# Optimization experiments

Hardware: AMD Instinct MI355X
Metric: run time of the kernel (lower is better)

Reference implementation:

```python
import jax, jax.numpy as jnp
import numpy as np
import math

DIM = 2048
N_HEADS = 16
Q_LORA = 512
KV_LORA = 512
NOPE = 128
ROPE = 64
QK_HD = NOPE + ROPE
V_HD = 128
THETA = 1e6


def _linear_params(key, fan_in, fan_out):
    kw, kb = jax.random.split(key)
    w = jax.random.normal(kw, (fan_in, fan_out), jnp.float32) * 0.02
    b = jax.random.normal(kb, (fan_out,), jnp.float32) * 0.02
    return w, b


def setup_inputs() -> dict:
    key = jax.random.key(0)
    ks = jax.random.split(key, 6)
    x = jax.random.normal(ks[0], (2, 2048, DIM), jnp.float32)
    wq_a_w, wq_a_b = _linear_params(ks[1], DIM, Q_LORA)
    wq_b_w, wq_b_b = _linear_params(ks[2], Q_LORA, N_HEADS * QK_HD)
    wkv_a_w, wkv_a_b = _linear_params(ks[3], DIM, KV_LORA + ROPE)
    wkv_b_w, wkv_b_b = _linear_params(ks[4], KV_LORA, N_HEADS * (NOPE + V_HD))
    wo_w, wo_b = _linear_params(ks[5], N_HEADS * V_HD, DIM)
    return {"x": x,
            "wq_a_w": wq_a_w, "wq_a_b": wq_a_b,
            "wq_b_w": wq_b_w, "wq_b_b": wq_b_b,
            "wkv_a_w": wkv_a_w, "wkv_a_b": wkv_a_b,
            "wkv_b_w": wkv_b_w, "wkv_b_b": wkv_b_b,
            "wo_w": wo_w, "wo_b": wo_b}


def _rope_cos_sin(seq_len):
    # freqs = 1/theta^(2i/ROPE), i in [0, ROPE/2)
    inv_freq = 1.0 / (THETA ** (jnp.arange(0, ROPE, 2, dtype=jnp.float32) / ROPE))
    t = jnp.arange(seq_len, dtype=jnp.float32)
    freqs = jnp.outer(t, inv_freq)  # (S, ROPE/2)
    return jnp.cos(freqs), jnp.sin(freqs)


def _apply_rope(x, cos, sin):
    # x: (B, S, H, ROPE); pairs (even, odd) form complex numbers
    xr = x[..., 0::2]
    xi = x[..., 1::2]
    c = cos[None, :, None, :]
    s = sin[None, :, None, :]
    out_r = xr * c - xi * s
    out_i = xr * s + xi * c
    return jnp.stack([out_r, out_i], axis=-1).reshape(x.shape)


def reference(x, wq_a_w, wq_a_b, wq_b_w, wq_b_b, wkv_a_w, wkv_a_b,
              wkv_b_w, wkv_b_b, wo_w, wo_b):
    bs, seq_len, _ = x.shape
    # low-rank Q projection
    q = (x @ wq_a_w + wq_a_b) @ wq_b_w + wq_b_b
    q = q.reshape(bs, seq_len, N_HEADS, QK_HD)
    q_nope, q_pe = q[..., :NOPE], q[..., NOPE:]
    # compressed KV + decoupled rope key
    ckv = x @ wkv_a_w + wkv_a_b
    compressed_kv, k_pe = ckv[..., :KV_LORA], ckv[..., KV_LORA:]
    k_pe = k_pe.reshape(bs, seq_len, 1, ROPE)
    kv = (compressed_kv @ wkv_b_w + wkv_b_b).reshape(bs, seq_len, N_HEADS, NOPE + V_HD)
    kv_nope, v = kv[..., :NOPE], kv[..., NOPE:]
    # partial RoPE
    cos, sin = _rope_cos_sin(seq_len)
    q_pe = _apply_rope(q_pe, cos, sin)
    k_pe = _apply_rope(k_pe, cos, sin)
    k_pe = jnp.broadcast_to(k_pe, (bs, seq_len, N_HEADS, ROPE))
    qf = jnp.concatenate([q_nope, q_pe], axis=-1)   # (B,S,H,QK_HD)
    kf = jnp.concatenate([kv_nope, k_pe], axis=-1)  # (B,S,H,QK_HD)
    # full attention (no mask, scale by sqrt(v_head_dim) per source)
    scores = jnp.einsum('bqhd,bkhd->bhqk', qf, kf) / math.sqrt(V_HD)
    probs = jax.nn.softmax(scores.astype(jnp.float32), axis=-1).astype(qf.dtype)
    out = jnp.einsum('bhqk,bkhd->bqhd', probs, v)
    out = out.reshape(bs, seq_len, N_HEADS * V_HD)
    return out @ wo_w + wo_b
```

## Files before the change

kernel.cpp:

```cpp
#include <hip/hip_runtime.h>
#include <hip/hip_bf16.h>


typedef __attribute__((ext_vector_type(8))) short short8;
typedef __attribute__((ext_vector_type(4))) short short4v;
typedef __attribute__((ext_vector_type(4))) float f32x4;

#define GLOAD_LDS16(gp, lp)                                                      \
  __builtin_amdgcn_global_load_lds((const __attribute__((address_space(1))) void*)(gp), \
                                   (__attribute__((address_space(3))) void*)(lp), 16, 0, 0)

static __device__ __forceinline__ unsigned short bf16_bits(float f) {
  __hip_bfloat16 h = __float2bfloat16(f);
  return __builtin_bit_cast(unsigned short, h);
}
static __device__ __forceinline__ float bf16_to_f(unsigned short u) {
  unsigned int v = (unsigned int)u << 16;
  return __builtin_bit_cast(float, v);
}


__global__ void k_f32_to_bf16(const float* __restrict__ in, unsigned short* __restrict__ out, int n4) {
  int i = blockIdx.x * 256 + threadIdx.x;
  if (i >= n4) return;
  float4 v = reinterpret_cast<const float4*>(in)[i];
  ushort4 o;
  o.x = bf16_bits(v.x); o.y = bf16_bits(v.y); o.z = bf16_bits(v.z); o.w = bf16_bits(v.w);
  reinterpret_cast<ushort4*>(out)[i] = o;
}

__global__ void k_transpose_bf16(const float* __restrict__ W, unsigned short* __restrict__ Wt,
                                 int K, int N) {
  __shared__ float tile[32][33];
  int k0 = blockIdx.x * 32, n0 = blockIdx.y * 32;
  int tx = threadIdx.x & 31, ty = threadIdx.x >> 5;
#pragma unroll
  for (int i = 0; i < 32; i += 8) {
    int k = k0 + ty + i, n = n0 + tx;
    tile[ty + i][tx] = (k < K && n < N) ? W[(size_t)k * N + n] : 0.f;
  }
  __syncthreads();
#pragma unroll
  for (int i = 0; i < 32; i += 8) {
    int n = n0 + ty + i, k = k0 + tx;
    if (n < N && k < K) Wt[(size_t)n * K + k] = bf16_bits(tile[tx][ty + i]);
  }
}


__global__ void k_rope_table(float2* __restrict__ cs) {
  int idx = blockIdx.x * 256 + threadIdx.x;
  int s = idx >> 5, i = idx & 31;
  float inv = powf(1.0e6f, -(float)(2 * i) / 64.0f);
  float a = (float)s * inv;
  cs[idx] = make_float2(cosf(a), sinf(a));
}

__global__ void k_rope_q(unsigned short* __restrict__ q, const float2* __restrict__ cs) {
  int idx = blockIdx.x * 256 + threadIdx.x;
  int i = idx & 31;
  int h = (idx >> 5) & 15;
  int bs = idx >> 9;
  int s = bs & 2047;
  size_t base = (size_t)bs * 3072 + h * 192 + 128 + 2 * i;
  float xr = bf16_to_f(q[base]);
  float xi = bf16_to_f(q[base + 1]);
  float2 c = cs[(s << 5) + i];
  q[base]     = bf16_bits(xr * c.x - xi * c.y);
  q[base + 1] = bf16_bits(xr * c.y + xi * c.x);
}

__global__ void k_rope_k(unsigned short* __restrict__ ckv, const float2* __restrict__ cs) {
  int idx = blockIdx.x * 256 + threadIdx.x;
  int i = idx & 31;
  int bs = idx >> 5;
  int s = bs & 2047;
  size_t base = (size_t)bs * 576 + 512 + 2 * i;
  float xr = bf16_to_f(ckv[base]);
  float xi = bf16_to_f(ckv[base + 1]);
  float2 c = cs[(s << 5) + i];
  ckv[base]     = bf16_bits(xr * c.x - xi * c.y);
  ckv[base + 1] = bf16_bits(xr * c.y + xi * c.x);
}


template <typename OutT>
__global__ __launch_bounds__(256, 2) void k_gemm(const unsigned short* __restrict__ A, int lda,
                                                 const unsigned short* __restrict__ Wt,
                                                 const float* __restrict__ bias,
                                                 OutT* __restrict__ C, int M, int N, int K) {
  __shared__ unsigned short lA[128][64];
  __shared__ unsigned short lB[128][64];
  int m0 = blockIdx.x * 128, n0 = blockIdx.y * 128;
  int t = threadIdx.x;
  int lane = t & 63, wid = t >> 6;
  int g = lane >> 4, col = lane & 15;
  int wr = wid >> 1, wc = wid & 1;
  int srow = lane >> 3;
  int schunk = (lane & 7) ^ srow;
  f32x4 acc[4][4] = {};

  for (int kt = 0; kt < K; kt += 64) {
#pragma unroll
    for (int i = 0; i < 4; ++i) {
      int rowb = 32 * wid + 8 * i;
      int row = rowb + srow;
      GLOAD_LDS16(&A[(size_t)(m0 + row) * lda + kt + 8 * schunk], &lA[rowb][0]);
      GLOAD_LDS16(&Wt[(size_t)(n0 + row) * K + kt + 8 * schunk], &lB[rowb][0]);
    }
    __syncthreads();
#pragma unroll
    for (int kk = 0; kk < 64; kk += 32) {
      int ch = (kk >> 3) + g;
      int sl = 8 * (ch ^ (col & 7));
      short8 a[4], b[4];
#pragma unroll
      for (int mf = 0; mf < 4; ++mf)
        a[mf] = *reinterpret_cast<const short8*>(&lA[64 * wr + 16 * mf + col][sl]);
#pragma unroll
      for (int nf = 0; nf < 4; ++nf)
        b[nf] = *reinterpret_cast<const short8*>(&lB[64 * wc + 16 * nf + col][sl]);
#pragma unroll
      for (int mf = 0; mf < 4; ++mf)
#pragma unroll
        for (int nf = 0; nf < 4; ++nf)
          acc[mf][nf] = __builtin_amdgcn_mfma_f32_16x16x32_bf16(a[mf], b[nf], acc[mf][nf], 0, 0, 0);
    }
    __syncthreads();
  }

#pragma unroll
  for (int mf = 0; mf < 4; ++mf) {
#pragma unroll
    for (int nf = 0; nf < 4; ++nf) {
      int n = n0 + 64 * wc + 16 * nf + col;
      if (n >= N) continue;
      float bv = bias[n];
#pragma unroll
      for (int r = 0; r < 4; ++r) {
        int m = m0 + 64 * wr + 16 * mf + 4 * g + r;
        float v = acc[mf][nf][r] + bv;
        if constexpr (sizeof(OutT) == 4)
          C[(size_t)m * N + n] = v;
        else
          C[(size_t)m * N + n] = bf16_bits(v);
      }
    }
  }
}


__global__ __launch_bounds__(512, 2) void k_attn(const unsigned short* __restrict__ q,
                                                 const unsigned short* __restrict__ ckv,
                                                 const unsigned short* __restrict__ kv,
                                                 unsigned short* __restrict__ out) {
  __shared__ unsigned short lK[64][200];
  __shared__ unsigned short lV[128][72];
  __shared__ unsigned short lP[8][32][72];
  int bx = blockIdx.x;
  int qt = bx & 7, h = (bx >> 3) & 15, b = bx >> 7;
  int t = threadIdx.x, lane = t & 63, w = t >> 6;
  int g = lane >> 4, col = lane & 15;
  int q0 = qt * 256;
  int bb = b * 2048;
  const float scale = 0.08838834764831845f;

  short8 qf[2][6];
#pragma unroll
  for (int m = 0; m < 2; ++m) {
    int srow = bb + q0 + 32 * w + 16 * m + col;
    size_t base = ((size_t)srow * 16 + h) * 192 + 8 * g;
#pragma unroll
    for (int j = 0; j < 6; ++j)
      qf[m][j] = *reinterpret_cast<const short8*>(&q[base + 32 * j]);
  }

  short8 kreg[3];
  short4v vreg0[2], vreg1[2];

  auto load_tile = [&](int k0) {
#pragma unroll
    for (int it = 0; it < 3; ++it) {
      int c = t + 512 * it;
      int row = c / 24, cc = c % 24;
      int s = bb + k0 + row;
      const unsigned short* src;
      if (cc < 16) src = &kv[((size_t)s * 16 + h) * 256 + cc * 8];
      else         src = &ckv[(size_t)s * 576 + 512 + (cc - 16) * 8];
      kreg[it] = *reinterpret_cast<const short8*>(src);
    }
#pragma unroll
    for (int it = 0; it < 2; ++it) {
      int c = t + 512 * it;
      int kp = c >> 5, dv0 = (c & 31) * 4;
      size_t vb = ((size_t)(bb + k0 + 2 * kp) * 16 + h) * 256 + 128 + dv0;
      vreg0[it] = *reinterpret_cast<const short4v*>(&kv[vb]);
      vreg1[it] = *reinterpret_cast<const short4v*>(&kv[vb + 4096]);
    }
  };

  load_tile(0);

  f32x4 o[2][8] = {};
  float mrow[2][4] = {{-1e30f, -1e30f, -1e30f, -1e30f}, {-1e30f, -1e30f, -1e30f, -1e30f}};
  float lrow[2][4] = {};

  for (int k0 = 0; k0 < 2048; k0 += 64) {
    __syncthreads();
#pragma unroll
    for (int it = 0; it < 3; ++it) {
      int c = t + 512 * it;
      int row = c / 24, cc = c % 24;
      *reinterpret_cast<short8*>(&lK[row][cc * 8]) = kreg[it];
    }
#pragma unroll
    for (int it = 0; it < 2; ++it) {
      int c = t + 512 * it;
      int kp = c >> 5, dv0 = (c & 31) * 4;
      int k2 = 2 * kp;
#pragma unroll
      for (int j = 0; j < 4; ++j) {
        int dv = dv0 + j;
        int phys = (((k2 >> 3) ^ ((dv >> 3) & 7)) << 3) + (k2 & 7);
        unsigned int pw = (unsigned int)(unsigned short)vreg0[it][j] |
                          ((unsigned int)(unsigned short)vreg1[it][j] << 16);
        *reinterpret_cast<unsigned int*>(&lV[dv][phys]) = pw;
      }
    }
    __syncthreads();
    if (k0 + 64 < 2048) load_tile(k0 + 64);
    __builtin_amdgcn_sched_barrier(0);

    f32x4 sf[2][4] = {};
    __builtin_amdgcn_s_setprio(1);
#pragma unroll
    for (int c = 0; c < 4; ++c) {
#pragma unroll
      for (int j = 0; j < 6; ++j) {
        short8 bfr = *reinterpret_cast<const short8*>(&lK[16 * c + col][32 * j + 8 * g]);
#pragma unroll
        for (int m = 0; m < 2; ++m)
          sf[m][c] = __builtin_amdgcn_mfma_f32_16x16x32_bf16(qf[m][j], bfr, sf[m][c], 0, 0, 0);
      }
    }
    __builtin_amdgcn_s_setprio(0);

#pragma unroll
    for (int m = 0; m < 2; ++m) {
#pragma unroll
      for (int r = 0; r < 4; ++r) {
        float tm = -1e30f;
#pragma unroll
        for (int c = 0; c < 4; ++c) { sf[m][c][r] *= scale; tm = fmaxf(tm, sf[m][c][r]); }
#pragma unroll
        for (int off = 8; off; off >>= 1) tm = fmaxf(tm, __shfl_xor(tm, off, 64));
        float mn = fmaxf(mrow[m][r], tm);
        float rs = __expf(mrow[m][r] - mn);
        mrow[m][r] = mn;
        float ps = 0.f;
#pragma unroll
        for (int c = 0; c < 4; ++c) { float p = __expf(sf[m][c][r] - mn); sf[m][c][r] = p; ps += p; }
#pragma unroll
        for (int off = 8; off; off >>= 1) ps += __shfl_xor(ps, off, 64);
        lrow[m][r] = lrow[m][r] * rs + ps;
#pragma unroll
        for (int n = 0; n < 8; ++n) o[m][n][r] *= rs;
      }
    }

#pragma unroll
    for (int m = 0; m < 2; ++m)
#pragma unroll
      for (int c = 0; c < 4; ++c)
#pragma unroll
        for (int r = 0; r < 4; ++r)
          lP[w][16 * m + 4 * g + r][16 * c + col] = bf16_bits(sf[m][c][r]);
    __builtin_amdgcn_s_setprio(1);
#pragma unroll
    for (int kk = 0; kk < 64; kk += 32) {
      short8 pa[2];
#pragma unroll
      for (int m = 0; m < 2; ++m)
        pa[m] = *reinterpret_cast<const short8*>(&lP[w][16 * m + col][kk + 8 * g]);
#pragma unroll
      for (int n = 0; n < 8; ++n) {
        int dv = 16 * n + col;
        int phys = ((((kk + 8 * g) >> 3) ^ ((dv >> 3) & 7)) << 3);
        short8 bv = *reinterpret_cast<const short8*>(&lV[dv][phys]);
#pragma unroll
        for (int m = 0; m < 2; ++m)
          o[m][n] = __builtin_amdgcn_mfma_f32_16x16x32_bf16(pa[m], bv, o[m][n], 0, 0, 0);
      }
    }
    __builtin_amdgcn_s_setprio(0);
  }

#pragma unroll
  for (int m = 0; m < 2; ++m) {
#pragma unroll
    for (int r = 0; r < 4; ++r) {
      float inv = 1.0f / lrow[m][r];
      int srow = bb + q0 + 32 * w + 16 * m + 4 * g + r;
      size_t base = (size_t)srow * 2048 + h * 128;
#pragma unroll
      for (int n = 0; n < 8; ++n)
        out[base + 16 * n + col] = bf16_bits(o[m][n][r] * inv);
    }
  }
}


extern "C" void kernel_launch(void* const* d_in, const int* in_sizes, int n_in,
                              void* d_out, int out_size, void* d_ws, size_t ws_size,
                              hipStream_t stream) {
  const float* x       = (const float*)d_in[0];
  const float* wq_a_w  = (const float*)d_in[1];
  const float* wq_a_b  = (const float*)d_in[2];
  const float* wq_b_w  = (const float*)d_in[3];
  const float* wq_b_b  = (const float*)d_in[4];
  const float* wkv_a_w = (const float*)d_in[5];
  const float* wkv_a_b = (const float*)d_in[6];
  const float* wkv_b_w = (const float*)d_in[7];
  const float* wkv_b_b = (const float*)d_in[8];
  const float* wo_w    = (const float*)d_in[9];
  const float* wo_b    = (const float*)d_in[10];
  float* out = (float*)d_out;

  const int BS = 4096;
  char* p = (char*)d_ws;
  auto alloc = [&](size_t bytes) { char* r = p; p += (bytes + 255) & ~(size_t)255; return r; };
  unsigned short* xb    = (unsigned short*)alloc((size_t)BS * 2048 * 2);
  unsigned short* wqat  = (unsigned short*)alloc((size_t)512 * 2048 * 2);
  unsigned short* wqbt  = (unsigned short*)alloc((size_t)3072 * 512 * 2);
  unsigned short* wkvat = (unsigned short*)alloc((size_t)640 * 2048 * 2);
  unsigned short* wkvbt = (unsigned short*)alloc((size_t)4096 * 512 * 2);
  unsigned short* wot   = (unsigned short*)alloc((size_t)2048 * 2048 * 2);
  unsigned short* qa    = (unsigned short*)alloc((size_t)BS * 512 * 2);
  unsigned short* qbuf  = (unsigned short*)alloc((size_t)BS * 3072 * 2);
  unsigned short* ckv   = (unsigned short*)alloc((size_t)BS * 576 * 2);
  unsigned short* kvbuf = (unsigned short*)alloc((size_t)BS * 4096 * 2);
  unsigned short* attno = (unsigned short*)alloc((size_t)BS * 2048 * 2);
  float2* cs            = (float2*)alloc((size_t)2048 * 32 * sizeof(float2));

  k_f32_to_bf16<<<BS * 2048 / 4 / 256, 256, 0, stream>>>(x, xb, BS * 2048 / 4);
  k_transpose_bf16<<<dim3(2048 / 32, 512 / 32), 256, 0, stream>>>(wq_a_w, wqat, 2048, 512);
  k_transpose_bf16<<<dim3(512 / 32, 3072 / 32), 256, 0, stream>>>(wq_b_w, wqbt, 512, 3072);
  k_transpose_bf16<<<dim3(2048 / 32, 576 / 32), 256, 0, stream>>>(wkv_a_w, wkvat, 2048, 576);
  k_transpose_bf16<<<dim3(512 / 32, 4096 / 32), 256, 0, stream>>>(wkv_b_w, wkvbt, 512, 4096);
  k_transpose_bf16<<<dim3(2048 / 32, 2048 / 32), 256, 0, stream>>>(wo_w, wot, 2048, 2048);
  k_rope_table<<<2048 * 32 / 256, 256, 0, stream>>>(cs);

  k_gemm<unsigned short><<<dim3(BS / 128, 512 / 128), 256, 0, stream>>>(
      xb, 2048, wqat, wq_a_b, qa, BS, 512, 2048);
  k_gemm<unsigned short><<<dim3(BS / 128, 3072 / 128), 256, 0, stream>>>(
      qa, 512, wqbt, wq_b_b, qbuf, BS, 3072, 512);
  k_gemm<unsigned short><<<dim3(BS / 128, (576 + 127) / 128), 256, 0, stream>>>(
      xb, 2048, wkvat, wkv_a_b, ckv, BS, 576, 2048);
  k_rope_q<<<BS * 16 * 32 / 256, 256, 0, stream>>>(qbuf, cs);
  k_rope_k<<<BS * 32 / 256, 256, 0, stream>>>(ckv, cs);
  k_gemm<unsigned short><<<dim3(BS / 128, 4096 / 128), 256, 0, stream>>>(
      ckv, 576, wkvbt, wkv_b_b, kvbuf, BS, 4096, 512);
  k_attn<<<2 * 16 * 8, 512, 0, stream>>>(qbuf, ckv, kvbuf, attno);
  k_gemm<float><<<dim3(BS / 128, 2048 / 128), 256, 0, stream>>>(
      attno, 2048, wot, wo_b, out, BS, 2048, 2048);
}
```

Before: 477.3 us.

## Fuse Q-down and KV-down projections into one GEMM; swizzle P tile and defer row-sum reduction

```diff
diff --git a/kernel.cpp b/kernel.cpp
--- a/kernel.cpp
+++ b/kernel.cpp
@@ -149,6 +149,69 @@
   }
 }
 
+__global__ __launch_bounds__(256, 2) void k_gemm_qkv(const unsigned short* __restrict__ A,
+                                                     const unsigned short* __restrict__ Wf,
+                                                     const float* __restrict__ biasf,
+                                                     unsigned short* __restrict__ qa,
+                                                     unsigned short* __restrict__ ckv) {
+  __shared__ unsigned short lA[128][64];
+  __shared__ unsigned short lB[128][64];
+  int m0 = blockIdx.x * 128, n0 = blockIdx.y * 128;
+  int t = threadIdx.x;
+  int lane = t & 63, wid = t >> 6;
+  int g = lane >> 4, col = lane & 15;
+  int wr = wid >> 1, wc = wid & 1;
+  int srow = lane >> 3;
+  int schunk = (lane & 7) ^ srow;
+  f32x4 acc[4][4] = {};
+
+  for (int kt = 0; kt < 2048; kt += 64) {
+#pragma unroll
+    for (int i = 0; i < 4; ++i) {
+      int rowb = 32 * wid + 8 * i;
+      int row = rowb + srow;
+      GLOAD_LDS16(&A[(size_t)(m0 + row) * 2048 + kt + 8 * schunk], &lA[rowb][0]);
+      GLOAD_LDS16(&Wf[(size_t)(n0 + row) * 2048 + kt + 8 * schunk], &lB[rowb][0]);
+    }
+    __syncthreads();
+#pragma unroll
+    for (int kk = 0; kk < 64; kk += 32) {
+      int ch = (kk >> 3) + g;
+      int sl = 8 * (ch ^ (col & 7));
+      short8 a[4], b[4];
+#pragma unroll
+      for (int mf = 0; mf < 4; ++mf)
+        a[mf] = *reinterpret_cast<const short8*>(&lA[64 * wr + 16 * mf + col][sl]);
+#pragma unroll
+      for (int nf = 0; nf < 4; ++nf)
+        b[nf] = *reinterpret_cast<const short8*>(&lB[64 * wc + 16 * nf + col][sl]);
+#pragma unroll
+      for (int mf = 0; mf < 4; ++mf)
+#pragma unroll
+        for (int nf = 0; nf < 4; ++nf)
+          acc[mf][nf] = __builtin_amdgcn_mfma_f32_16x16x32_bf16(a[mf], b[nf], acc[mf][nf], 0, 0, 0);
+    }
+    __syncthreads();
+  }
+
+#pragma unroll
+  for (int mf = 0; mf < 4; ++mf) {
+#pragma unroll
+    for (int nf = 0; nf < 4; ++nf) {
+      int n = n0 + 64 * wc + 16 * nf + col;
+      if (n >= 1088) continue;
+      float bv = biasf[n];
+#pragma unroll
+      for (int r = 0; r < 4; ++r) {
+        int m = m0 + 64 * wr + 16 * mf + 4 * g + r;
+        float v = acc[mf][nf][r] + bv;
+        if (n < 512) qa[(size_t)m * 512 + n] = bf16_bits(v);
+        else         ckv[(size_t)m * 576 + (n - 512)] = bf16_bits(v);
+      }
+    }
+  }
+}
+
 
 __global__ __launch_bounds__(512, 2) void k_attn(const unsigned short* __restrict__ q,
                                                  const unsigned short* __restrict__ ckv,
@@ -260,8 +323,6 @@
         float ps = 0.f;
 #pragma unroll
         for (int c = 0; c < 4; ++c) { float p = __expf(sf[m][c][r] - mn); sf[m][c][r] = p; ps += p; }
-#pragma unroll
-        for (int off = 8; off; off >>= 1) ps += __shfl_xor(ps, off, 64);
         lrow[m][r] = lrow[m][r] * rs + ps;
 #pragma unroll
         for (int n = 0; n < 8; ++n) o[m][n][r] *= rs;
@@ -273,15 +334,22 @@
 #pragma unroll
       for (int c = 0; c < 4; ++c)
 #pragma unroll
-        for (int r = 0; r < 4; ++r)
-          lP[w][16 * m + 4 * g + r][16 * c + col] = bf16_bits(sf[m][c][r]);
+        for (int r = 0; r < 4; ++r) {
+          int rowp = 16 * m + 4 * g + r;
+          int k16 = 16 * c + col;
+          int phys = ((((k16 >> 3) ^ ((rowp >> 2) & 7))) << 3) + (k16 & 7);
+          lP[w][rowp][phys] = bf16_bits(sf[m][c][r]);
+        }
     __builtin_amdgcn_s_setprio(1);
 #pragma unroll
     for (int kk = 0; kk < 64; kk += 32) {
       short8 pa[2];
 #pragma unroll
-      for (int m = 0; m < 2; ++m)
-        pa[m] = *reinterpret_cast<const short8*>(&lP[w][16 * m + col][kk + 8 * g]);
+      for (int m = 0; m < 2; ++m) {
+        int rowp = 16 * m + col;
+        int ck = ((kk + 8 * g) >> 3) ^ ((rowp >> 2) & 7);
+        pa[m] = *reinterpret_cast<const short8*>(&lP[w][rowp][ck << 3]);
+      }
 #pragma unroll
       for (int n = 0; n < 8; ++n) {
         int dv = 16 * n + col;
@@ -299,7 +367,10 @@
   for (int m = 0; m < 2; ++m) {
 #pragma unroll
     for (int r = 0; r < 4; ++r) {
-      float inv = 1.0f / lrow[m][r];
+      float tot = lrow[m][r];
+#pragma unroll
+      for (int off = 8; off; off >>= 1) tot += __shfl_xor(tot, off, 64);
+      float inv = 1.0f / tot;
       int srow = bb + q0 + 32 * w + 16 * m + 4 * g + r;
       size_t base = (size_t)srow * 2048 + h * 128;
 #pragma unroll
@@ -329,33 +400,33 @@
   const int BS = 4096;
   char* p = (char*)d_ws;
   auto alloc = [&](size_t bytes) { char* r = p; p += (bytes + 255) & ~(size_t)255; return r; };
-  unsigned short* xb    = (unsigned short*)alloc((size_t)BS * 2048 * 2);
-  unsigned short* wqat  = (unsigned short*)alloc((size_t)512 * 2048 * 2);
-  unsigned short* wqbt  = (unsigned short*)alloc((size_t)3072 * 512 * 2);
-  unsigned short* wkvat = (unsigned short*)alloc((size_t)640 * 2048 * 2);
-  unsigned short* wkvbt = (unsigned short*)alloc((size_t)4096 * 512 * 2);
-  unsigned short* wot   = (unsigned short*)alloc((size_t)2048 * 2048 * 2);
-  unsigned short* qa    = (unsigned short*)alloc((size_t)BS * 512 * 2);
-  unsigned short* qbuf  = (unsigned short*)alloc((size_t)BS * 3072 * 2);
-  unsigned short* ckv   = (unsigned short*)alloc((size_t)BS * 576 * 2);
-  unsigned short* kvbuf = (unsigned short*)alloc((size_t)BS * 4096 * 2);
-  unsigned short* attno = (unsigned short*)alloc((size_t)BS * 2048 * 2);
-  float2* cs            = (float2*)alloc((size_t)2048 * 32 * sizeof(float2));
+  unsigned short* xb     = (unsigned short*)alloc((size_t)BS * 2048 * 2);
+  unsigned short* wfused = (unsigned short*)alloc((size_t)1152 * 2048 * 2);
+  unsigned short* wqbt   = (unsigned short*)alloc((size_t)3072 * 512 * 2);
+  unsigned short* wkvbt  = (unsigned short*)alloc((size_t)4096 * 512 * 2);
+  unsigned short* wot    = (unsigned short*)alloc((size_t)2048 * 2048 * 2);
+  float* biasf           = (float*)alloc((size_t)1152 * sizeof(float));
+  unsigned short* qa     = (unsigned short*)alloc((size_t)BS * 512 * 2);
+  unsigned short* qbuf   = (unsigned short*)alloc((size_t)BS * 3072 * 2);
+  unsigned short* ckv    = (unsigned short*)alloc((size_t)BS * 576 * 2);
+  unsigned short* kvbuf  = (unsigned short*)alloc((size_t)BS * 4096 * 2);
+  unsigned short* attno  = (unsigned short*)alloc((size_t)BS * 2048 * 2);
+  float2* cs             = (float2*)alloc((size_t)2048 * 32 * sizeof(float2));
 
   k_f32_to_bf16<<<BS * 2048 / 4 / 256, 256, 0, stream>>>(x, xb, BS * 2048 / 4);
-  k_transpose_bf16<<<dim3(2048 / 32, 512 / 32), 256, 0, stream>>>(wq_a_w, wqat, 2048, 512);
+  k_transpose_bf16<<<dim3(2048 / 32, 512 / 32), 256, 0, stream>>>(wq_a_w, wfused, 2048, 512);
+  k_transpose_bf16<<<dim3(2048 / 32, 576 / 32), 256, 0, stream>>>(
+      wkv_a_w, wfused + (size_t)512 * 2048, 2048, 576);
   k_transpose_bf16<<<dim3(512 / 32, 3072 / 32), 256, 0, stream>>>(wq_b_w, wqbt, 512, 3072);
-  k_transpose_bf16<<<dim3(2048 / 32, 576 / 32), 256, 0, stream>>>(wkv_a_w, wkvat, 2048, 576);
   k_transpose_bf16<<<dim3(512 / 32, 4096 / 32), 256, 0, stream>>>(wkv_b_w, wkvbt, 512, 4096);
   k_transpose_bf16<<<dim3(2048 / 32, 2048 / 32), 256, 0, stream>>>(wo_w, wot, 2048, 2048);
   k_rope_table<<<2048 * 32 / 256, 256, 0, stream>>>(cs);
-
-  k_gemm<unsigned short><<<dim3(BS / 128, 512 / 128), 256, 0, stream>>>(
-      xb, 2048, wqat, wq_a_b, qa, BS, 512, 2048);
+  hipMemcpyAsync(biasf, wq_a_b, 512 * sizeof(float), hipMemcpyDeviceToDevice, stream);
+  hipMemcpyAsync(biasf + 512, wkv_a_b, 576 * sizeof(float), hipMemcpyDeviceToDevice, stream);
+
+  k_gemm_qkv<<<dim3(BS / 128, 9), 256, 0, stream>>>(xb, wfused, biasf, qa, ckv);
   k_gemm<unsigned short><<<dim3(BS / 128, 3072 / 128), 256, 0, stream>>>(
       qa, 512, wqbt, wq_b_b, qbuf, BS, 3072, 512);
-  k_gemm<unsigned short><<<dim3(BS / 128, (576 + 127) / 128), 256, 0, stream>>>(
-      xb, 2048, wkvat, wkv_a_b, ckv, BS, 576, 2048);
   k_rope_q<<<BS * 16 * 32 / 256, 256, 0, stream>>>(qbuf, cs);
   k_rope_k<<<BS * 32 / 256, 256, 0, stream>>>(ckv, cs);
   k_gemm<unsigned short><<<dim3(BS / 128, 4096 / 128), 256, 0, stream>>>(
```

Measured after the change: 407.3 us. 14.7% less time.
